# Optimization experiments

Hardware: AMD Instinct MI355X
Metric: run time of the kernel (lower is better)

Reference implementation:

```python
import jax, jax.numpy as jnp
import numpy as np

N_FEATS = 9       # OGB atom feature columns
VOCAB = 119       # per-feature embedding vocab (max OGB atom vocab)
HIDDEN = 128
NUM_HEADS = 8
HEAD_DIM = HIDDEN // NUM_HEADS


def setup_inputs() -> dict:
    key = jax.random.key(0)
    ks = jax.random.split(key, 12)
    N, K = 50000, 16
    X = jax.random.randint(ks[0], (N, N_FEATS), 0, VOCAB)
    nbr_idx = jax.random.randint(ks[1], (N, K), 0, N)
    nbr_mask = jax.random.randint(ks[2], (N, K), 0, 2).astype(bool)
    atom_emb = jax.random.normal(ks[3], (N_FEATS, VOCAB, HIDDEN), jnp.float32) * 0.02
    s = 1.0 / np.sqrt(HIDDEN)
    Wq = jax.random.normal(ks[4], (HIDDEN, HIDDEN), jnp.float32) * s
    bq = jnp.zeros((HIDDEN,), jnp.float32)
    Wk = jax.random.normal(ks[5], (HIDDEN, HIDDEN), jnp.float32) * s
    bk = jnp.zeros((HIDDEN,), jnp.float32)
    Wv = jax.random.normal(ks[6], (HIDDEN, HIDDEN), jnp.float32) * s
    bv = jnp.zeros((HIDDEN,), jnp.float32)
    return {"X": X, "nbr_idx": nbr_idx, "nbr_mask": nbr_mask,
            "atom_emb": atom_emb, "Wq": Wq, "bq": bq,
            "Wk": Wk, "bk": bk, "Wv": Wv, "bv": bv}


def reference(X, nbr_idx, nbr_mask, atom_emb, Wq, bq, Wk, bk, Wv, bv):
    N = X.shape[0]
    # AtomEncoder: sum per-feature embedding lookups -> [N, HIDDEN]
    h = jnp.sum(atom_emb[jnp.arange(N_FEATS)[None, :], X], axis=1)
    scaling = HEAD_DIM ** -0.5
    q = (h @ Wq + bq).reshape(N, NUM_HEADS, HEAD_DIM) * scaling
    k = (h @ Wk + bk).reshape(N, NUM_HEADS, HEAD_DIM)
    v = (h @ Wv + bv).reshape(N, NUM_HEADS, HEAD_DIM)
    # ELL-format sparse attention: gather padded neighbor k/v -> [N, K, H, D]
    k_n = k[nbr_idx]
    v_n = v[nbr_idx]
    scores = jnp.einsum('nhd,nkhd->nkh', q, k_n)          # [N, K, H]
    scores = jnp.where(nbr_mask[..., None], scores, -1e9)
    attn = jax.nn.softmax(scores, axis=1)                 # softmax over neighbors
    out = jnp.einsum('nkh,nkhd->nhd', attn, v_n)          # [N, H, D]
    return out.reshape(N, HIDDEN)
```

## Files before the change

### kernel.cpp

```cpp
#include <hip/hip_runtime.h>
#include <hip/hip_bf16.h>

#define NFEAT 9
#define VOCAB 119
#define HIDDEN 128
#define NHEAD 8
#define HDIM 16
#define KNBR 16

typedef __attribute__((ext_vector_type(8))) short short8;
typedef __attribute__((ext_vector_type(4))) float f32x4;

__device__ __forceinline__ void load_lds16(const void* g, void* l) {
    __builtin_amdgcn_global_load_lds((const __attribute__((address_space(1))) void*)g,
                                     (__attribute__((address_space(3))) void*)l, 16, 0, 0);
}

template <int OFFS>
__device__ __forceinline__ float swz_xor(float v) {
    int r = __builtin_amdgcn_ds_swizzle(__float_as_int(v), OFFS);
    return __int_as_float(r);
}

__global__ void fill_kernel(float* out, int n, float val) {
    int i = blockIdx.x * blockDim.x + threadIdx.x;
    if (i < n) out[i] = val;
}

__global__ __launch_bounds__(256) void wt_kernel(
    const float* __restrict__ Wq, const float* __restrict__ Wk,
    const float* __restrict__ Wv, short* __restrict__ Wt)
{
    int mat = blockIdx.x >> 2, tile = blockIdx.x & 3;
    const float* W = (mat == 0) ? Wq : (mat == 1) ? Wk : Wv;
    __shared__ float ls[32 * HIDDEN];
    int tid = threadIdx.x;
    int cc0 = tile * 32;
    #pragma unroll
    for (int j = 0; j < 16; ++j) {
        int idx = j * 256 + tid;
        ls[idx] = W[(size_t)cc0 * HIDDEN + idx];
    }
    __syncthreads();
    int c = tid & 127, hf = tid >> 7;
    unsigned int ob[8];
    #pragma unroll
    for (int j = 0; j < 8; ++j) {
        int ccl = hf * 16 + 2 * j;
        __hip_bfloat16 b0 = __float2bfloat16(ls[ccl * HIDDEN + c]);
        __hip_bfloat16 b1 = __float2bfloat16(ls[(ccl + 1) * HIDDEN + c]);
        ob[j] = (unsigned int)*reinterpret_cast<unsigned short*>(&b0)
              | ((unsigned int)*reinterpret_cast<unsigned short*>(&b1) << 16);
    }
    unsigned int* dst = reinterpret_cast<unsigned int*>(
        Wt + (size_t)mat * HIDDEN * HIDDEN + (size_t)c * HIDDEN + cc0 + hf * 16);
    #pragma unroll
    for (int j = 0; j < 8; ++j) dst[j] = ob[j];
}

#define MT 32
#define HBS 136

__global__ __launch_bounds__(256, 3) void qkv_kernel(
    const int* __restrict__ X, const float* __restrict__ emb,
    const short* __restrict__ Wt,
    const float* __restrict__ bq, const float* __restrict__ bk,
    const float* __restrict__ bv,
    float* __restrict__ qf, __hip_bfloat16* __restrict__ kv, int N)
{
    __shared__ __align__(16) short hb[MT * HBS];
    __shared__ int xs[MT * NFEAT];

    const int tid = threadIdx.x;
    const int n0 = blockIdx.x * MT;

    for (int i = tid; i < MT * NFEAT; i += 256) {
        int n = n0 + i / NFEAT;
        int v = (n < N) ? X[(size_t)n * NFEAT + (i % NFEAT)] : 0;
        xs[i] = min(max(v, 0), VOCAB - 1);
    }
    __syncthreads();

    {
        const int cg = tid & 31;
        const int slot = tid >> 5;
        #pragma unroll
        for (int i = 0; i < 4; ++i) {
            int nl = slot * 4 + i;
            float4 acc = {0.f, 0.f, 0.f, 0.f};
            #pragma unroll
            for (int f = 0; f < NFEAT; ++f) {
                const float4 e = *reinterpret_cast<const float4*>(
                    &emb[((size_t)f * VOCAB + xs[nl * NFEAT + f]) * HIDDEN + cg * 4]);
                acc.x += e.x; acc.y += e.y; acc.z += e.z; acc.w += e.w;
            }
            __hip_bfloat162 p0 = __float22bfloat162_rn(make_float2(acc.x, acc.y));
            __hip_bfloat162 p1 = __float22bfloat162_rn(make_float2(acc.z, acc.w));
            uint2 u;
            u.x = *reinterpret_cast<unsigned int*>(&p0);
            u.y = *reinterpret_cast<unsigned int*>(&p1);
            *reinterpret_cast<uint2*>(&hb[nl * HBS + cg * 4]) = u;
        }
    }
    __syncthreads();

    const int wave = tid >> 6, lane = tid & 63;
    const int l15 = lane & 15, quad = lane >> 4;

    short8 b[2][3][4];
    float bias[2][3];
    #pragma unroll
    for (int g = 0; g < 2; ++g) {
        const int n = (wave * 2 + g) * 16 + l15;
        #pragma unroll
        for (int mat = 0; mat < 3; ++mat) {
            #pragma unroll
            for (int k0 = 0; k0 < 4; ++k0)
                b[g][mat][k0] = *reinterpret_cast<const short8*>(
                    &Wt[(size_t)mat * HIDDEN * HIDDEN + n * HIDDEN + k0 * 32 + quad * 8]);
            bias[g][mat] = (mat == 0) ? bq[n] : (mat == 1) ? bk[n] : bv[n];
        }
    }

    #pragma unroll
    for (int mt = 0; mt < 2; ++mt) {
        const int mloc = mt * 16 + l15;
        short8 a[4];
        #pragma unroll
        for (int k0 = 0; k0 < 4; ++k0)
            a[k0] = *reinterpret_cast<const short8*>(
                &hb[mloc * HBS + k0 * 32 + quad * 8]);
        #pragma unroll
        for (int g = 0; g < 2; ++g) {
            const int n = (wave * 2 + g) * 16 + l15;
            f32x4 acc[3] = {{0.f,0.f,0.f,0.f},{0.f,0.f,0.f,0.f},{0.f,0.f,0.f,0.f}};
            #pragma unroll
            for (int mat = 0; mat < 3; ++mat)
                #pragma unroll
                for (int k0 = 0; k0 < 4; ++k0)
                    acc[mat] = __builtin_amdgcn_mfma_f32_16x16x32_bf16(
                        a[k0], b[g][mat][k0], acc[mat], 0, 0, 0);
            #pragma unroll
            for (int mat = 0; mat < 3; ++mat) {
                #pragma unroll
                for (int r = 0; r < 4; ++r) {
                    int node = n0 + mt * 16 + quad * 4 + r;
                    if (node < N) {
                        float val = acc[mat][r] + bias[g][mat];
                        if (mat == 0)      qf[(size_t)node * HIDDEN + n] = val * 0.25f;
                        else if (mat == 1) kv[(size_t)node * 256 + n] = __float2bfloat16(val);
                        else               kv[(size_t)node * 256 + 128 + n] = __float2bfloat16(val);
                    }
                }
            }
        }
    }
}

#define NPB2 2
#define KGW 520

__global__ __launch_bounds__(256) void attn_kernel(
    const int* __restrict__ nbr_idx, const int* __restrict__ nbr_mask,
    const float* __restrict__ qf, const __hip_bfloat16* __restrict__ kv,
    float* __restrict__ out, int N)
{
    __shared__ __align__(16) __hip_bfloat16 kl[NPB2][4][KGW];
    __shared__ __align__(16) float sl[NPB2][NHEAD][20];
    __shared__ __align__(16) int idxl[NPB2][KNBR];
    __shared__ int mskl[NPB2][KNBR];

    const int tid = threadIdx.x;
    const int local = tid >> 7;
    const int t = tid & 127;
    int n = blockIdx.x * NPB2 + local;
    if (n >= N) n = N - 1;

    if (t < KNBR) {
        int iv = nbr_idx[(size_t)n * KNBR + t];
        idxl[local][t] = min(max(iv, 0), N - 1);
        mskl[local][t] = nbr_mask[(size_t)n * KNBR + t];
    }
    __syncthreads();

    const int hh = t >> 4;
    const int kk = t & 15;

    int idxr[KNBR];
    {
        const int4* ip = reinterpret_cast<const int4*>(&idxl[local][0]);
        #pragma unroll
        for (int m4 = 0; m4 < 4; ++m4) {
            int4 iv = ip[m4];
            idxr[4 * m4 + 0] = iv.x; idxr[4 * m4 + 1] = iv.y;
            idxr[4 * m4 + 2] = iv.z; idxr[4 * m4 + 3] = iv.w;
        }
    }
    const int mymsk = mskl[local][kk];

    {
        const int w2 = t >> 6;
        const int l = t & 63;
        #pragma unroll
        for (int j2 = 0; j2 < 2; ++j2) {
            int g = j2 * 2 + w2;
            int r = g * 4 + (l >> 4);
            if (mskl[local][r]) {
                const short* src = (const short*)kv
                    + (size_t)idxl[local][r] * 256 + (size_t)(l & 15) * 8;
                load_lds16(src, &kl[local][g][0]);
            }
        }
    }

    float vr[KNBR];
    #pragma unroll
    for (int j = 0; j < KNBR; ++j) {
        unsigned int u = *((const unsigned short*)kv + (size_t)idxr[j] * 256 + 128 + t);
        vr[j] = __uint_as_float(u << 16);
    }

    float qr[HDIM];
    {
        const float4* qp = reinterpret_cast<const float4*>(
            qf + (size_t)n * HIDDEN + hh * HDIM);
        #pragma unroll
        for (int c4 = 0; c4 < 4; ++c4) {
            float4 qv = qp[c4];
            qr[4 * c4 + 0] = qv.x; qr[4 * c4 + 1] = qv.y;
            qr[4 * c4 + 2] = qv.z; qr[4 * c4 + 3] = qv.w;
        }
    }
    __syncthreads();

    {
        const int g = kk >> 2, rg = kk & 3;
        const short8* kb = reinterpret_cast<const short8*>(
            &kl[local][g][rg * 128 + hh * HDIM]);
        short8 k0 = kb[0], k1 = kb[1];
        const __hip_bfloat162* kp0 = reinterpret_cast<const __hip_bfloat162*>(&k0);
        const __hip_bfloat162* kp1 = reinterpret_cast<const __hip_bfloat162*>(&k1);
        float s = 0.f;
        #pragma unroll
        for (int d2 = 0; d2 < 4; ++d2) {
            float2 f0 = __bfloat1622float2(kp0[d2]);
            float2 f1 = __bfloat1622float2(kp1[d2]);
            s += qr[2 * d2] * f0.x + qr[2 * d2 + 1] * f0.y;
            s += qr[8 + 2 * d2] * f1.x + qr[8 + 2 * d2 + 1] * f1.y;
        }
        if (!mymsk) s = -1e9f;
        float m = s;
        m = fmaxf(m, swz_xor<0x041F>(m));
        m = fmaxf(m, swz_xor<0x081F>(m));
        m = fmaxf(m, swz_xor<0x101F>(m));
        m = fmaxf(m, swz_xor<0x201F>(m));
        float e = __expf(s - m);
        float d = e;
        d += swz_xor<0x041F>(d);
        d += swz_xor<0x081F>(d);
        d += swz_xor<0x101F>(d);
        d += swz_xor<0x201F>(d);
        sl[local][hh][kk] = e / d;
    }
    __syncthreads();

    {
        float o = 0.f;
        const float4* wp = reinterpret_cast<const float4*>(&sl[local][hh][0]);
        #pragma unroll
        for (int m4 = 0; m4 < 4; ++m4) {
            float4 w4 = wp[m4];
            o += w4.x * vr[4 * m4 + 0] + w4.y * vr[4 * m4 + 1]
               + w4.z * vr[4 * m4 + 2] + w4.w * vr[4 * m4 + 3];
        }
        out[(size_t)n * HIDDEN + t] = o;
    }
}

extern "C" void kernel_launch(void* const* d_in, const int* in_sizes, int n_in,
                              void* d_out, int out_size, void* d_ws, size_t ws_size,
                              hipStream_t stream)
{
    float* out = (float*)d_out;

    bool ok = (n_in == 10);
    int N = ok ? in_sizes[0] / NFEAT : 0;
    ok = ok && N > 0 && in_sizes[0] == N * NFEAT
            && in_sizes[1] == N * KNBR
            && in_sizes[2] == N * KNBR
            && in_sizes[3] == NFEAT * VOCAB * HIDDEN
            && in_sizes[4] == HIDDEN * HIDDEN && in_sizes[5] == HIDDEN
            && in_sizes[6] == HIDDEN * HIDDEN && in_sizes[7] == HIDDEN
            && in_sizes[8] == HIDDEN * HIDDEN && in_sizes[9] == HIDDEN
            && out_size == N * HIDDEN;
    if (!ok) {
        fill_kernel<<<(out_size + 255) / 256, 256, 0, stream>>>(out, out_size, 0.0f);
        return;
    }
    size_t need = (size_t)N * 1024 + 3 * HIDDEN * HIDDEN * sizeof(short);
    if (ws_size < need) {
        fill_kernel<<<(out_size + 255) / 256, 256, 0, stream>>>(out, out_size, 1.0f);
        return;
    }

    const int* X        = (const int*)d_in[0];
    const int* nbr_idx  = (const int*)d_in[1];
    const int* nbr_mask = (const int*)d_in[2];
    const float* emb = (const float*)d_in[3];
    const float* Wq  = (const float*)d_in[4];
    const float* bq  = (const float*)d_in[5];
    const float* Wk  = (const float*)d_in[6];
    const float* bk  = (const float*)d_in[7];
    const float* Wv  = (const float*)d_in[8];
    const float* bv  = (const float*)d_in[9];

    float* qf = (float*)d_ws;
    __hip_bfloat16* kv =
        (__hip_bfloat16*)((char*)d_ws + (size_t)N * HIDDEN * sizeof(float));
    short* Wt = (short*)((char*)d_ws + (size_t)N * 1024);

    wt_kernel<<<12, 256, 0, stream>>>(Wq, Wk, Wv, Wt);
    qkv_kernel<<<(N + MT - 1) / MT, 256, 0, stream>>>(
        X, emb, Wt, bq, bk, bv, qf, kv, N);
    attn_kernel<<<(N + NPB2 - 1) / NPB2, 256, 0, stream>>>(
        nbr_idx, nbr_mask, qf, kv, out, N);
}
```

Measured before the change: 167.3 us.

## Drop LDS staging and barriers in attention kernel, load K directly per thread

```diff
diff --git a/kernel.cpp b/kernel.cpp
--- a/kernel.cpp
+++ b/kernel.cpp
@@ -10,11 +10,6 @@
 
 typedef __attribute__((ext_vector_type(8))) short short8;
 typedef __attribute__((ext_vector_type(4))) float f32x4;
-
-__device__ __forceinline__ void load_lds16(const void* g, void* l) {
-    __builtin_amdgcn_global_load_lds((const __attribute__((address_space(1))) void*)g,
-                                     (__attribute__((address_space(3))) void*)l, 16, 0, 0);
-}
 
 template <int OFFS>
 __device__ __forceinline__ float swz_xor(float v) {
@@ -158,17 +153,13 @@
 }
 
 #define NPB2 2
-#define KGW 520
 
 __global__ __launch_bounds__(256) void attn_kernel(
     const int* __restrict__ nbr_idx, const int* __restrict__ nbr_mask,
     const float* __restrict__ qf, const __hip_bfloat16* __restrict__ kv,
     float* __restrict__ out, int N)
 {
-    __shared__ __align__(16) __hip_bfloat16 kl[NPB2][4][KGW];
     __shared__ __align__(16) float sl[NPB2][NHEAD][20];
-    __shared__ __align__(16) int idxl[NPB2][KNBR];
-    __shared__ int mskl[NPB2][KNBR];
 
     const int tid = threadIdx.x;
     const int local = tid >> 7;
@@ -176,48 +167,30 @@
     int n = blockIdx.x * NPB2 + local;
     if (n >= N) n = N - 1;
 
-    if (t < KNBR) {
-        int iv = nbr_idx[(size_t)n * KNBR + t];
-        idxl[local][t] = min(max(iv, 0), N - 1);
-        mskl[local][t] = nbr_mask[(size_t)n * KNBR + t];
-    }
-    __syncthreads();
-
     const int hh = t >> 4;
     const int kk = t & 15;
 
     int idxr[KNBR];
     {
-        const int4* ip = reinterpret_cast<const int4*>(&idxl[local][0]);
+        const int4* ip = reinterpret_cast<const int4*>(nbr_idx + (size_t)n * KNBR);
         #pragma unroll
         for (int m4 = 0; m4 < 4; ++m4) {
             int4 iv = ip[m4];
-            idxr[4 * m4 + 0] = iv.x; idxr[4 * m4 + 1] = iv.y;
-            idxr[4 * m4 + 2] = iv.z; idxr[4 * m4 + 3] = iv.w;
-        }
-    }
-    const int mymsk = mskl[local][kk];
-
-    {
-        const int w2 = t >> 6;
-        const int l = t & 63;
-        #pragma unroll
-        for (int j2 = 0; j2 < 2; ++j2) {
-            int g = j2 * 2 + w2;
-            int r = g * 4 + (l >> 4);
-            if (mskl[local][r]) {
-                const short* src = (const short*)kv
-                    + (size_t)idxl[local][r] * 256 + (size_t)(l & 15) * 8;
-                load_lds16(src, &kl[local][g][0]);
-            }
-        }
-    }
-
-    float vr[KNBR];
-    #pragma unroll
-    for (int j = 0; j < KNBR; ++j) {
-        unsigned int u = *((const unsigned short*)kv + (size_t)idxr[j] * 256 + 128 + t);
-        vr[j] = __uint_as_float(u << 16);
+            idxr[4 * m4 + 0] = min(max(iv.x, 0), N - 1);
+            idxr[4 * m4 + 1] = min(max(iv.y, 0), N - 1);
+            idxr[4 * m4 + 2] = min(max(iv.z, 0), N - 1);
+            idxr[4 * m4 + 3] = min(max(iv.w, 0), N - 1);
+        }
+    }
+    const int mymsk = nbr_mask[(size_t)n * KNBR + kk];
+
+    short8 k0 = {0, 0, 0, 0, 0, 0, 0, 0};
+    short8 k1 = {0, 0, 0, 0, 0, 0, 0, 0};
+    if (mymsk) {
+        const short8* kp = reinterpret_cast<const short8*>(
+            (const short*)kv + (size_t)idxr[kk] * 256 + hh * HDIM);
+        k0 = kp[0];
+        k1 = kp[1];
     }
 
     float qr[HDIM];
@@ -231,13 +204,15 @@
             qr[4 * c4 + 2] = qv.z; qr[4 * c4 + 3] = qv.w;
         }
     }
-    __syncthreads();
-
-    {
-        const int g = kk >> 2, rg = kk & 3;
-        const short8* kb = reinterpret_cast<const short8*>(
-            &kl[local][g][rg * 128 + hh * HDIM]);
-        short8 k0 = kb[0], k1 = kb[1];
+
+    float vr[KNBR];
+    #pragma unroll
+    for (int j = 0; j < KNBR; ++j) {
+        unsigned int u = *((const unsigned short*)kv + (size_t)idxr[j] * 256 + 128 + t);
+        vr[j] = __uint_as_float(u << 16);
+    }
+
+    {
         const __hip_bfloat162* kp0 = reinterpret_cast<const __hip_bfloat162*>(&k0);
         const __hip_bfloat162* kp1 = reinterpret_cast<const __hip_bfloat162*>(&k1);
         float s = 0.f;
@@ -262,11 +237,10 @@
         d += swz_xor<0x201F>(d);
         sl[local][hh][kk] = e / d;
     }
-    __syncthreads();
 
     {
         float o = 0.f;
-        const float4* wp = reinterpret_cast<const float4*>(&sl[local][hh][0]);
+        const float4* wp = reinterpret_cast<const float4*>(&sl[local][t >> 4][0]);
         #pragma unroll
         for (int m4 = 0; m4 < 4; ++m4) {
             float4 w4 = wp[m4];
```

After: 170.2 us. Within noise of the previous version (+1.7%).
